# Performance work log

Measured on AMD Instinct MI355X. Metric: run time of the kernel, lower is better.

## Reference

```python
import jax, jax.numpy as jnp
import numpy as np

N = 512          # octave output grid resolution per cube side
M = 256          # input octave resolution
FACTOR = 0.5     # 2 ** (-factor), factor = 1
EPS = 1e-12


def make_cube_faces(n):
    # two triangles per quad on each of the 6 n x n side grids
    idx = np.arange(n * n).reshape(n, n)
    a = idx[:-1, :-1].ravel(); b = idx[:-1, 1:].ravel()
    c = idx[1:, :-1].ravel(); d = idx[1:, 1:].ravel()
    tris = np.concatenate([np.stack([a, b, c], 1), np.stack([b, d, c], 1)], 0)
    faces = np.concatenate([tris + s * n * n for s in range(6)], 0)
    return jnp.asarray(faces, jnp.int32)  # [F, 3]


def to_stacked(t):
    # [1, 6*m*m, 3] -> [6, 3, m, m]
    m = int(round((t.shape[1] // 6) ** 0.5))
    return t.reshape(6, m, m, 3).transpose(0, 3, 1, 2)


def to_vertices(s):
    # [6, 3, m, m] -> [1, 6*m*m, 3]
    return s.transpose(0, 2, 3, 1).reshape(1, -1, 3)


def resize_bilinear_ac(t, n):
    # bilinear, align_corners=True, square input [.., m, m] -> [.., n, n]
    m = t.shape[-1]
    coords = jnp.linspace(0.0, m - 1.0, n)
    i0 = jnp.clip(jnp.floor(coords).astype(jnp.int32), 0, m - 1)
    i1 = jnp.minimum(i0 + 1, m - 1)
    w = (coords - i0).astype(t.dtype)
    t = t[..., i0, :] * (1.0 - w)[:, None] + t[..., i1, :] * w[:, None]
    t = t[..., :, i0] * (1.0 - w) + t[..., :, i1] * w
    return t


def compute_face_normals(vert, faces):
    v = vert[0]                                  # [V, 3]
    v0, v1, v2 = v[faces[:, 0]], v[faces[:, 1]], v[faces[:, 2]]
    fn = jnp.cross(v1 - v0, v2 - v0)             # [F, 3]
    nrm = jnp.linalg.norm(fn, axis=-1, keepdims=True)
    return fn / jnp.maximum(nrm, EPS)


def compute_vertex_normals(vert, faces, face_normals):
    V = vert.shape[1]
    flat_idx = faces.reshape(-1)                          # [3F] f0v0,f0v1,f0v2,...
    rep = jnp.repeat(face_normals, 3, axis=0)             # [3F, 3]
    acc = jax.ops.segment_sum(rep, flat_idx, num_segments=V)  # scatter-add
    nrm = jnp.linalg.norm(acc, axis=-1, keepdims=True)
    return (acc / jnp.maximum(nrm, EPS))[None]            # [1, V, 3]


def get_vertex_normals(vert, faces):
    fn = compute_face_normals(vert, faces)
    normals = compute_vertex_normals(vert, faces, fn)
    stacked = to_stacked(normals)                         # [6, 3, n, n]
    sign = jnp.array([-1.0, 1.0, 1.0, -1.0, -1.0, 1.0], stacked.dtype)
    stacked = stacked * sign[:, None, None, None]
    return to_vertices(stacked)


def setup_inputs() -> dict:
    key = jax.random.key(0)
    k1, k2 = jax.random.split(key)
    vrt = jax.random.normal(k1, (1, 6 * M * M, 3), jnp.float32)
    nrm = jax.random.normal(k2, (1, 6 * M * M, 3), jnp.float32)
    ps = jnp.zeros((6, 1, N, N), jnp.float32)   # nn.Parameter(zeros * noise)
    faces = make_cube_faces(N)
    return {"vrt": vrt, "nrm": nrm, "ps": ps, "faces": faces}


def reference(vrt, nrm, ps, faces):
    vrt_s = resize_bilinear_ac(to_stacked(vrt), N)                 # [6,3,n,n]
    nrm_mag = jnp.linalg.norm(resize_bilinear_ac(to_stacked(nrm), N),
                              axis=1, keepdims=True)               # [6,1,n,n]
    stacked = vrt_s + FACTOR * jax.nn.sigmoid(ps) * nrm_mag
    vert = to_vertices(stacked)                                    # [1, V, 3]
    normals = get_vertex_normals(vert, faces)
    return vert, faces, normals
```

## Files before the change

kernel.cpp:

```cpp
#include <hip/hip_runtime.h>
#include <math.h>

#define NSZ 512
#define MSZ 256
#define NPIX (6 * NSZ * NSZ)
#define NQu  261121u
#define NQ2u 522242u
#define NFACE 3133452
#define F3TOT 9400356
#define NFT12 783363
#define TS 32
#define HS 34
#define QS 33
#define NVB 1536
#define NFB ((NFT12 + 255) / 256)
#define GRID (NVB + NFB)

typedef __fp16 h2_t __attribute__((ext_vector_type(2)));

__device__ inline float fast_rcp(float x) {
    float r = __builtin_amdgcn_rcpf(x);
    return r * (2.0f - x * r);
}
__device__ inline float fast_rsqrt(float d) {
    float r = __builtin_amdgcn_rsqf(d);
    return r * (1.5f - 0.5f * d * r * r);
}
__device__ inline float fast_sigmoid(float x) {
    float e = __builtin_amdgcn_exp2f(-1.442695040888963f * x);
    return fast_rcp(1.0f + e);
}
__device__ inline float lerpf(float a, float b, float w) {
    return __builtin_fmaf(w, b - a, a);
}
__device__ inline unsigned pkh2(float x, float y) {
    h2_t h = __builtin_amdgcn_cvt_pkrtz(x, y);
    return __builtin_bit_cast(unsigned, h);
}
__device__ inline float2 uph2(unsigned u) {
    h2_t h = __builtin_bit_cast(h2_t, u);
    return make_float2((float)h.x, (float)h.y);
}

__global__ __launch_bounds__(256) void k_all(const float* __restrict__ vrt,
                                             const float* __restrict__ nrm,
                                             const float* __restrict__ ps,
                                             float* __restrict__ out0,
                                             float* __restrict__ out1,
                                             float* __restrict__ out2) {
    __shared__ float sv[HS * HS * 3];
    __shared__ unsigned tnXY0[QS * QS];
    __shared__ unsigned tnXY1[QS * QS];
    __shared__ unsigned tnZZ [QS * QS];

    int blk = blockIdx.x;

    if (blk >= NVB) {
        int t = (blk - NVB) * 256 + threadIdx.x;
        if (t >= NFT12) return;
        unsigned tri = 4u * (unsigned)t;
        unsigned s   = tri / NQ2u;
        unsigned r1  = tri - s * NQ2u;
        unsigned ty  = (r1 >= NQu) ? 1u : 0u;
        unsigned qi  = r1 - ty * NQu;
        unsigned R   = qi / 511u;
        unsigned Q   = qi - R * 511u;

        unsigned a[4], tt[4];
        unsigned aq = Q, aR = R, aty = ty, as_ = s;
#pragma unroll
        for (int k = 0; k < 4; ++k) {
            a[k]  = (as_ << 18) + (aR << 9) + aq;
            tt[k] = aty;
            aq++;
            if (aq == 511u) {
                aq = 0u; aR++;
                if (aR == 511u) { aR = 0u; aty ^= 1u; if (aty == 0u) as_++; }
            }
        }
        float w[12];
#pragma unroll
        for (int k = 0; k < 4; ++k) {
            w[3*k + 0] = (float)(a[k] + (tt[k] ? 1u : 0u));
            w[3*k + 1] = (float)(a[k] + (tt[k] ? 513u : 1u));
            w[3*k + 2] = (float)(a[k] + 512u);
        }
        float4* o = (float4*)out1 + 3 * t;
        o[0] = make_float4(w[0], w[1], w[2],  w[3]);
        o[1] = make_float4(w[4], w[5], w[6],  w[7]);
        o[2] = make_float4(w[8], w[9], w[10], w[11]);
        return;
    }

    int f   = blk >> 8;
    int tl  = blk & 255;
    int tr  = (tl >> 4) * TS;
    int tq  = (tl & 15) * TS;
    int fbm = f * (MSZ * MSZ);
    int fbn = f * (NSZ * NSZ);
    const float scale = 255.0f / 511.0f;

    auto vert_item = [&](int p) {
        int pr = p / HS, pq = p - pr * HS;
        int y = tr + pr - 1, x = tq + pq - 1;
        int yc = min(max(y, 0), NSZ - 1);
        int xc = min(max(x, 0), NSZ - 1);

        float cy = (float)yc * scale;
        float cx = (float)xc * scale;
        int iy0 = min((int)cy, MSZ - 1);
        int ix0 = min((int)cx, MSZ - 1);
        float wy = cy - (float)iy0;
        float wx = cx - (float)ix0;
        int   iya = min(iy0, MSZ - 2);
        int   ixa = min(ix0, MSZ - 2);
        float wya = (iy0 < MSZ - 1) ? wy : 1.0f;
        float wxa = (ix0 < MSZ - 1) ? wx : 1.0f;

        int g0 = (fbm + iya * MSZ + ixa) * 3;
        int g1 = g0 + MSZ * 3;

        float vx, vy, vz;
        {
            float a0 = vrt[g0], a1 = vrt[g0+1], a2 = vrt[g0+2];
            float a3 = vrt[g0+3], a4 = vrt[g0+4], a5 = vrt[g0+5];
            float b0 = vrt[g1], b1 = vrt[g1+1], b2 = vrt[g1+2];
            float b3 = vrt[g1+3], b4 = vrt[g1+4], b5 = vrt[g1+5];
            vx = lerpf(lerpf(a0, a3, wxa), lerpf(b0, b3, wxa), wya);
            vy = lerpf(lerpf(a1, a4, wxa), lerpf(b1, b4, wxa), wya);
            vz = lerpf(lerpf(a2, a5, wxa), lerpf(b2, b5, wxa), wya);
        }
        float nx, ny, nz;
        {
            float a0 = nrm[g0], a1 = nrm[g0+1], a2 = nrm[g0+2];
            float a3 = nrm[g0+3], a4 = nrm[g0+4], a5 = nrm[g0+5];
            float b0 = nrm[g1], b1 = nrm[g1+1], b2 = nrm[g1+2];
            float b3 = nrm[g1+3], b4 = nrm[g1+4], b5 = nrm[g1+5];
            nx = lerpf(lerpf(a0, a3, wxa), lerpf(b0, b3, wxa), wya);
            ny = lerpf(lerpf(a1, a4, wxa), lerpf(b1, b4, wxa), wya);
            nz = lerpf(lerpf(a2, a5, wxa), lerpf(b2, b5, wxa), wya);
        }

        float mag = __builtin_amdgcn_sqrtf(nx * nx + ny * ny + nz * nz);
        float sig = fast_sigmoid(ps[fbn + yc * NSZ + xc]);
        float add = 0.5f * sig * mag;
        float ox = vx + add, oy = vy + add, oz = vz + add;

        sv[p * 3 + 0] = ox;
        sv[p * 3 + 1] = oy;
        sv[p * 3 + 2] = oz;
        if (pr >= 1 && pr <= TS && pq >= 1 && pq <= TS) {
            int gi = (fbn + y * NSZ + x) * 3;
            out0[gi + 0] = ox;
            out0[gi + 1] = oy;
            out0[gi + 2] = oz;
        }
    };
    {
        int tid = threadIdx.x;
#pragma unroll
        for (int k = 0; k < 4; ++k) vert_item(tid + 256 * k);
        if (tid < HS * HS - 1024) vert_item(tid + 1024);
    }
    __syncthreads();

    auto quad_item = [&](int p) {
        int Ri = p / QS, Qi = p - Ri * QS;
        int base = (Ri * HS + Qi) * 3;
        float Axx = sv[base + 0],        Axy = sv[base + 1],        Axz = sv[base + 2];
        float Bxx = sv[base + 3],        Bxy = sv[base + 4],        Bxz = sv[base + 5];
        float Cxx = sv[base + HS*3 + 0], Cxy = sv[base + HS*3 + 1], Cxz = sv[base + HS*3 + 2];
        float Dxx = sv[base + HS*3 + 3], Dxy = sv[base + HS*3 + 4], Dxz = sv[base + HS*3 + 5];

        float n0x, n0y, n0z;
        {
            float e1x = Bxx - Axx, e1y = Bxy - Axy, e1z = Bxz - Axz;
            float e2x = Cxx - Axx, e2y = Cxy - Axy, e2z = Cxz - Axz;
            float cx = e1y * e2z - e1z * e2y;
            float cy = e1z * e2x - e1x * e2z;
            float cz = e1x * e2y - e1y * e2x;
            float d  = fmaxf(cx * cx + cy * cy + cz * cz, 1e-24f);
            float r  = fast_rsqrt(d);
            n0x = cx * r; n0y = cy * r; n0z = cz * r;
        }
        float n1x, n1y, n1z;
        {
            float e1x = Dxx - Bxx, e1y = Dxy - Bxy, e1z = Dxz - Bxz;
            float e2x = Cxx - Bxx, e2y = Cxy - Bxy, e2z = Cxz - Bxz;
            float cx = e1y * e2z - e1z * e2y;
            float cy = e1z * e2x - e1x * e2z;
            float cz = e1x * e2y - e1y * e2x;
            float d  = fmaxf(cx * cx + cy * cy + cz * cz, 1e-24f);
            float r  = fast_rsqrt(d);
            n1x = cx * r; n1y = cy * r; n1z = cz * r;
        }
        tnXY0[p] = pkh2(n0x, n0y);
        tnXY1[p] = pkh2(n1x, n1y);
        tnZZ [p] = pkh2(n0z, n1z);
    };
    {
        int tid = threadIdx.x;
#pragma unroll
        for (int k = 0; k < 4; ++k) quad_item(tid + 256 * k);
        if (tid < QS * QS - 1024) quad_item(tid + 1024);
    }
    __syncthreads();

    float sg = (f == 1 || f == 2 || f == 5) ? 1.0f : -1.0f;
    auto norm_item = [&](int p) {
        int r = p >> 5, q = p & 31;
        int q00 = r * QS + q;
        int q01 = q00 + 1;
        int q10 = q00 + QS;
        int q11 = q10 + 1;

        float2 a0 = uph2(tnXY0[q11]);
        float2 a1 = uph2(tnXY0[q10]);
        float2 a2 = uph2(tnXY0[q01]);
        float2 b0 = uph2(tnXY1[q10]);
        float2 b1 = uph2(tnXY1[q00]);
        float2 b2 = uph2(tnXY1[q01]);
        float2 zA = uph2(tnZZ[q11]);
        float2 zB = uph2(tnZZ[q10]);
        float2 zC = uph2(tnZZ[q01]);
        float2 zD = uph2(tnZZ[q00]);

        float ax = a0.x + a1.x + a2.x + b0.x + b1.x + b2.x;
        float ay = a0.y + a1.y + a2.y + b0.y + b1.y + b2.y;
        float az = zA.x + zB.x + zC.x + zB.y + zD.y + zC.y;

        float d  = fmaxf(ax * ax + ay * ay + az * az, 1e-24f);
        float rs = fast_rsqrt(d) * sg;
        int gi = (fbn + (tr + r) * NSZ + (tq + q)) * 3;
        out2[gi + 0] = ax * rs;
        out2[gi + 1] = ay * rs;
        out2[gi + 2] = az * rs;
    };
    {
        int tid = threadIdx.x;
#pragma unroll
        for (int k = 0; k < 4; ++k) norm_item(tid + 256 * k);
    }
}

extern "C" void kernel_launch(void* const* d_in, const int* in_sizes, int n_in,
                              void* d_out, int out_size, void* d_ws, size_t ws_size,
                              hipStream_t stream) {
    const float* vrt = (const float*)d_in[0];
    const float* nrm = (const float*)d_in[1];
    const float* ps  = (const float*)d_in[2];

    float* out0 = (float*)d_out;
    float* out1 = out0 + (size_t)NPIX * 3;
    float* out2 = out1 + (size_t)F3TOT;

    k_all<<<GRID, 256, 0, stream>>>(vrt, nrm, ps, out0, out1, out2);
}
```

Measured before the change: 26.58 us.

## Use nontemporal stores and register-blocked 4-wide vertex normal output

Output writes for faces, vertices and normals switch to nontemporal stores so write-once data bypasses cache retention. The vertex normal stage now has each thread handle four consecutive pixels in a row. It reuses a 5-wide window of packed face normals from shared memory in registers and writes three 16-byte vector stores instead of scalar strided stores. This cuts LDS reads and store instruction count, at the cost of more registers per thread.

```diff
diff --git a/kernel.cpp b/kernel.cpp
--- a/kernel.cpp
+++ b/kernel.cpp
@@ -17,6 +17,7 @@
 #define GRID (NVB + NFB)
 
 typedef __fp16 h2_t __attribute__((ext_vector_type(2)));
+typedef float  f4_t __attribute__((ext_vector_type(4)));
 
 __device__ inline float fast_rcp(float x) {
     float r = __builtin_amdgcn_rcpf(x);
@@ -40,6 +41,10 @@
 __device__ inline float2 uph2(unsigned u) {
     h2_t h = __builtin_bit_cast(h2_t, u);
     return make_float2((float)h.x, (float)h.y);
+}
+__device__ inline void nt_store4(f4_t* p, float a, float b, float c, float d) {
+    f4_t v = {a, b, c, d};
+    __builtin_nontemporal_store(v, p);
 }
 
 __global__ __launch_bounds__(256) void k_all(const float* __restrict__ vrt,
@@ -85,10 +90,10 @@
             w[3*k + 1] = (float)(a[k] + (tt[k] ? 513u : 1u));
             w[3*k + 2] = (float)(a[k] + 512u);
         }
-        float4* o = (float4*)out1 + 3 * t;
-        o[0] = make_float4(w[0], w[1], w[2],  w[3]);
-        o[1] = make_float4(w[4], w[5], w[6],  w[7]);
-        o[2] = make_float4(w[8], w[9], w[10], w[11]);
+        f4_t* o = (f4_t*)out1 + 3 * t;
+        nt_store4(o + 0, w[0], w[1], w[2],  w[3]);
+        nt_store4(o + 1, w[4], w[5], w[6],  w[7]);
+        nt_store4(o + 2, w[8], w[9], w[10], w[11]);
         return;
     }
 
@@ -150,10 +155,10 @@
         sv[p * 3 + 1] = oy;
         sv[p * 3 + 2] = oz;
         if (pr >= 1 && pr <= TS && pq >= 1 && pq <= TS) {
-            int gi = (fbn + y * NSZ + x) * 3;
-            out0[gi + 0] = ox;
-            out0[gi + 1] = oy;
-            out0[gi + 2] = oz;
+            float* gp = &out0[(size_t)(fbn + y * NSZ + x) * 3];
+            __builtin_nontemporal_store(ox, gp + 0);
+            __builtin_nontemporal_store(oy, gp + 1);
+            __builtin_nontemporal_store(oz, gp + 2);
         }
     };
     {
@@ -207,39 +212,51 @@
     __syncthreads();
 
     float sg = (f == 1 || f == 2 || f == 5) ? 1.0f : -1.0f;
-    auto norm_item = [&](int p) {
-        int r = p >> 5, q = p & 31;
-        int q00 = r * QS + q;
-        int q01 = q00 + 1;
-        int q10 = q00 + QS;
-        int q11 = q10 + 1;
-
-        float2 a0 = uph2(tnXY0[q11]);
-        float2 a1 = uph2(tnXY0[q10]);
-        float2 a2 = uph2(tnXY0[q01]);
-        float2 b0 = uph2(tnXY1[q10]);
-        float2 b1 = uph2(tnXY1[q00]);
-        float2 b2 = uph2(tnXY1[q01]);
-        float2 zA = uph2(tnZZ[q11]);
-        float2 zB = uph2(tnZZ[q10]);
-        float2 zC = uph2(tnZZ[q01]);
-        float2 zD = uph2(tnZZ[q00]);
-
-        float ax = a0.x + a1.x + a2.x + b0.x + b1.x + b2.x;
-        float ay = a0.y + a1.y + a2.y + b0.y + b1.y + b2.y;
-        float az = zA.x + zB.x + zC.x + zB.y + zD.y + zC.y;
-
-        float d  = fmaxf(ax * ax + ay * ay + az * az, 1e-24f);
-        float rs = fast_rsqrt(d) * sg;
-        int gi = (fbn + (tr + r) * NSZ + (tq + q)) * 3;
-        out2[gi + 0] = ax * rs;
-        out2[gi + 1] = ay * rs;
-        out2[gi + 2] = az * rs;
-    };
     {
-        int tid = threadIdx.x;
-#pragma unroll
-        for (int k = 0; k < 4; ++k) norm_item(tid + 256 * k);
+        int r  = threadIdx.x >> 3;
+        int q0 = (threadIdx.x & 7) * 4;
+        int b0 = r * QS + q0;
+        int b1 = b0 + QS;
+
+        unsigned t0r0[5], t0r1[5], t1r0[5], t1r1[5], zr0[5], zr1[5];
+#pragma unroll
+        for (int c = 0; c < 5; ++c) {
+            t0r0[c] = tnXY0[b0 + c];
+            t0r1[c] = tnXY0[b1 + c];
+            t1r0[c] = tnXY1[b0 + c];
+            t1r1[c] = tnXY1[b1 + c];
+            zr0[c]  = tnZZ [b0 + c];
+            zr1[c]  = tnZZ [b1 + c];
+        }
+
+        float ov[12];
+#pragma unroll
+        for (int i = 0; i < 4; ++i) {
+            float2 a0 = uph2(t0r1[i + 1]);
+            float2 a1 = uph2(t0r1[i]);
+            float2 a2 = uph2(t0r0[i + 1]);
+            float2 c0 = uph2(t1r1[i]);
+            float2 c1 = uph2(t1r0[i]);
+            float2 c2 = uph2(t1r0[i + 1]);
+            float2 zA = uph2(zr1[i + 1]);
+            float2 zB = uph2(zr1[i]);
+            float2 zC = uph2(zr0[i + 1]);
+            float2 zD = uph2(zr0[i]);
+
+            float ax = a0.x + a1.x + a2.x + c0.x + c1.x + c2.x;
+            float ay = a0.y + a1.y + a2.y + c0.y + c1.y + c2.y;
+            float az = zA.x + zB.x + zC.x + zB.y + zD.y + zC.y;
+
+            float d  = fmaxf(ax * ax + ay * ay + az * az, 1e-24f);
+            float rs = fast_rsqrt(d) * sg;
+            ov[3*i + 0] = ax * rs;
+            ov[3*i + 1] = ay * rs;
+            ov[3*i + 2] = az * rs;
+        }
+        f4_t* o = (f4_t*)&out2[(size_t)(fbn + (tr + r) * NSZ + tq + q0) * 3];
+        nt_store4(o + 0, ov[0], ov[1], ov[2],  ov[3]);
+        nt_store4(o + 1, ov[4], ov[5], ov[6],  ov[7]);
+        nt_store4(o + 2, ov[8], ov[9], ov[10], ov[11]);
     }
 }
 
```

Result: slower. 60.13 us (+126.2%).
